# Kernel optimization log

Hardware: AMD Instinct MI355X
Metric: run time of the kernel (lower is better)

## Reference

```python
import jax, jax.numpy as jnp
import numpy as np

B, CIN, H, W = 4, 2048, 65, 65
NC, INNER, QL = 19, 256, 2975
TEMP = 0.2
EPS = 1e-5


def _conv(x, w, dil=1, pad=0):
    return jax.lax.conv_general_dilated(
        x, w, (1, 1), [(pad, pad), (pad, pad)], rhs_dilation=(dil, dil),
        dimension_numbers=('NCHW', 'OIHW', 'NCHW'))


def _bn_relu(x, g, b):
    # training-mode BatchNorm2d (batch statistics over N,H,W) + ReLU
    m = x.mean(axis=(0, 2, 3), keepdims=True)
    v = x.var(axis=(0, 2, 3), keepdims=True)
    return jax.nn.relu(g[None, :, None, None] * (x - m) * jax.lax.rsqrt(v + EPS)
                       + b[None, :, None, None])


def setup_inputs() -> dict:
    key = jax.random.key(0)
    ks = jax.random.split(key, 12)
    rn = lambda k, s, sc=0.02: jax.random.normal(k, s, jnp.float32) * sc
    inp = {
        'x': jax.random.normal(ks[0], (B, CIN, H, W), jnp.float32),
        # ASPP: global-pool branch (1x1), 1x1 branch, three dilated 3x3 branches
        'w_gp': rn(ks[1], (INNER, CIN, 1, 1)), 'g_gp': jnp.ones(INNER), 'b_gp': jnp.zeros(INNER),
        'w_1x1': rn(ks[2], (INNER, CIN, 1, 1)), 'g_1x1': jnp.ones(INNER), 'b_1x1': jnp.zeros(INNER),
        'w_d12': rn(ks[3], (INNER, CIN, 3, 3)), 'g_d12': jnp.ones(INNER), 'b_d12': jnp.zeros(INNER),
        'w_d24': rn(ks[4], (INNER, CIN, 3, 3)), 'g_d24': jnp.ones(INNER), 'b_d24': jnp.zeros(INNER),
        'w_d36': rn(ks[5], (INNER, CIN, 3, 3)), 'g_d36': jnp.ones(INNER), 'b_d36': jnp.zeros(INNER),
        # head: 3x3 conv on 5*INNER concat -> 256, BN, ReLU (Dropout2d = identity)
        'w_head': rn(ks[6], (256, 5 * INNER, 3, 3)), 'g_head': jnp.ones(256), 'b_head': jnp.zeros(256),
        # final 1x1 classifier
        'w_fin': rn(ks[7], (NC, 256, 1, 1)), 'b_fin': jnp.zeros(NC),
    }
    q = jax.random.normal(ks[8], (NC, INNER, QL), jnp.float32)
    inp['queues'] = q / jnp.linalg.norm(q, axis=1, keepdims=True)  # normalize dim=0 per-class
    return inp


def reference(x, w_gp, g_gp, b_gp, w_1x1, g_1x1, b_1x1,
              w_d12, g_d12, b_d12, w_d24, g_d24, b_d24, w_d36, g_d36, b_d36,
              w_head, g_head, b_head, w_fin, b_fin, queues):
    bsz = x.shape[0]
    # ---- ASPP ----
    gp = x.mean(axis=(2, 3), keepdims=True)                       # global avg pool
    br0 = _bn_relu(_conv(gp, w_gp), g_gp, b_gp)
    br0 = jnp.broadcast_to(br0, (bsz, INNER, x.shape[2], x.shape[3]))
    br1 = _bn_relu(_conv(x, w_1x1), g_1x1, b_1x1)
    br2 = _bn_relu(_conv(x, w_d12, 12, 12), g_d12, b_d12)
    br3 = _bn_relu(_conv(x, w_d24, 24, 24), g_d24, b_d24)
    br4 = _bn_relu(_conv(x, w_d36, 36, 36), g_d36, b_d36)
    aspp_out = jnp.concatenate([br0, br1, br2, br3, br4], axis=1)  # (B, 5*INNER, H, W)
    # ---- head + final (Dropout2d(0.1) treated as identity) ----
    fea = _bn_relu(_conv(aspp_out, w_head, 1, 1), g_head, b_head)  # (B, 256, H, W)
    res = _conv(fea, w_fin) + b_fin[None, :, None, None]           # (B, NC, H, W)
    # ---- construct_region: per-class masked mean over ALL batch pixels ----
    pred = jnp.argmax(res, axis=1).reshape(bsz, -1)                # (B, HW)
    onehot = (pred[:, None, :] == jnp.arange(NC)[None, :, None]).astype(fea.dtype)  # (B,NC,HW)
    feaf = fea.reshape(bsz, 256, -1)                               # (B, 256, HW)
    sums = jnp.einsum('bcp,bkp->kc', feaf, onehot)                 # (NC, 256)
    counts = onehot.sum(axis=(0, 2))                               # (NC,)
    keys = sums / jnp.maximum(counts, 1.0)[:, None]
    keys = keys / jnp.maximum(jnp.linalg.norm(keys, axis=1, keepdims=True), 1e-12)
    present = counts > 0
    # ---- contrast loss: (query . queue)/INNER == mean over channels ----
    sims = jnp.einsum('kc,jcl->kjl', keys, jax.lax.stop_gradient(queues)) / INNER  # (NC,NC,QL)
    a = sims / TEMP
    lse_rows = jax.nn.logsumexp(a, axis=2)                         # (NC, NC)
    neg_rows = jnp.where(jnp.eye(NC, dtype=bool), -jnp.inf, lse_rows)
    lse_neg = jax.nn.logsumexp(neg_rows, axis=1)                   # (NC,) lse over 18*QL negatives
    pos = a[jnp.arange(NC), jnp.arange(NC)]                        # (NC, QL) diagonal class sims
    # CE with label 0 over [pos_i, negs] == logaddexp(pos_i, lse_neg) - pos_i, averaged over QL
    loss_per = (jnp.logaddexp(pos, lse_neg[:, None]) - pos).mean(axis=1)
    contrast_loss = jnp.sum(jnp.where(present, loss_per, 0.0))
    return res, contrast_loss
```

## Files before the change

kernel.cpp:

```cpp
#include <hip/hip_runtime.h>
#include <stdint.h>

#define HW_   4225
#define NPIX_ 16900
#define NC_   19
#define QL_   2975
#define EPSF  1e-5f

typedef __bf16 bf16x8 __attribute__((ext_vector_type(8)));
typedef float  f32x4  __attribute__((ext_vector_type(4)));

__device__ __forceinline__ unsigned short f2bf(float f) {
    union { float f; unsigned u; } v; v.f = f;
    unsigned u = v.u;
    return (unsigned short)((u + 0x7fffu + ((u >> 16) & 1u)) >> 16);
}
__device__ __forceinline__ float bf2f(unsigned short b) {
    union { unsigned u; float f; } v; v.u = ((unsigned)b) << 16;
    return v.f;
}

__global__ void k_transpose_x(const float* __restrict__ x, unsigned short* __restrict__ xt) {
    __shared__ unsigned short T[64][66];
    int b  = blockIdx.z;
    int c0 = blockIdx.y * 64;
    int p0 = blockIdx.x * 64;
    int tx = threadIdx.x & 63, ty = threadIdx.x >> 6;
    if (p0 + tx < HW_) {
        #pragma unroll
        for (int i = 0; i < 16; ++i) {
            int cl = i * 4 + ty;
            T[cl][tx] = f2bf(x[((size_t)(b * 2048 + c0 + cl)) * HW_ + p0 + tx]);
        }
    }
    __syncthreads();
    #pragma unroll
    for (int i = 0; i < 16; ++i) {
        int pl = i * 4 + ty;
        int p = p0 + pl;
        if (p < HW_) xt[((size_t)(b * HW_ + p)) * 2048 + c0 + tx] = T[tx][pl];
    }
}

__global__ void k_gp(const float* __restrict__ x, float* __restrict__ gp) {
    int wid  = blockIdx.x * 4 + (threadIdx.x >> 6);
    int lane = threadIdx.x & 63;
    int b = wid >> 11, c = wid & 2047;
    const float* src = x + (size_t)(b * 2048 + c) * HW_;
    float s = 0.f;
    for (int i = lane; i < HW_; i += 64) s += src[i];
    #pragma unroll
    for (int off = 32; off; off >>= 1) s += __shfl_down(s, off);
    if (lane == 0) gp[b * 2048 + c] = s * (1.0f / HW_);
}

__global__ void k_wreorder(const float* __restrict__ src, unsigned short* __restrict__ dst,
                           int ci_n, int ntaps) {
    int ci  = blockIdx.x * 256 + threadIdx.x;
    int co  = blockIdx.y, tap = blockIdx.z;
    dst[((size_t)tap * 256 + co) * ci_n + ci] =
        f2bf(src[((size_t)co * ci_n + ci) * ntaps + tap]);
}

__global__ __launch_bounds__(256) void k_conv_gemm(
    const unsigned short* __restrict__ xin, const unsigned short* __restrict__ wr_base,
    unsigned short* __restrict__ out, int cin, int ostride, int is_head)
{
    __shared__ unsigned short As[128 * 72];
    __shared__ unsigned short Bs[128 * 72];
    const int tid = threadIdx.x;
    const int bz = blockIdx.z;
    int dil, ntaps, coff;
    if (is_head) { dil = 1; ntaps = 9; coff = 0; }
    else         { dil = 12 * bz; ntaps = bz ? 9 : 1; coff = 256 * (bz + 1); }
    const int mbase = blockIdx.x * 128;
    const int nbase = blockIdx.y * 128;

    const int srow = tid >> 1;
    const int scol = (tid & 1) << 5;

    const int pix = mbase + srow;
    const int pb = pix / HW_;
    const int pr = pix - pb * HW_;
    const int py = pr / 65;
    const int px = pr - py * 65;

    f32x4 acc[4][4];
    #pragma unroll
    for (int i = 0; i < 4; ++i)
        #pragma unroll
        for (int j = 0; j < 4; ++j) acc[i][j] = (f32x4){0.f, 0.f, 0.f, 0.f};

    const int wv = tid >> 6, lane = tid & 63;
    const int wm = wv >> 1, wn = wv & 1;
    const int quad = lane >> 4, lrow = lane & 15;

    for (int tap = 0; tap < ntaps; ++tap) {
        int dy = (ntaps == 1) ? 0 : (tap / 3 - 1) * dil;
        int dx = (ntaps == 1) ? 0 : (tap % 3 - 1) * dil;
        int ys = py + dy, xs = px + dx;
        bool valid = (pix < NPIX_) && ((unsigned)ys < 65u) && ((unsigned)xs < 65u);
        size_t aoff = valid ? ((size_t)(pb * HW_ + ys * 65 + xs) * cin + scol) : 0;
        const unsigned short* asrc = xin + aoff;
        const unsigned short* bsrc = wr_base +
            ((size_t)(bz * 9 + tap) * 256 + (nbase + srow)) * cin + scol;

        for (int kc = 0; kc < cin; kc += 64) {
            uint4 a0, a1, a2, a3;
            if (valid) {
                const uint4* ap = (const uint4*)(asrc + kc);
                a0 = ap[0]; a1 = ap[1]; a2 = ap[2]; a3 = ap[3];
            } else {
                a0 = a1 = a2 = a3 = make_uint4(0u, 0u, 0u, 0u);
            }
            const uint4* bp = (const uint4*)(bsrc + kc);
            uint4 b0 = bp[0], b1 = bp[1], b2 = bp[2], b3 = bp[3];
            __syncthreads();
            uint4* ad = (uint4*)(As + srow * 72 + scol);
            ad[0] = a0; ad[1] = a1; ad[2] = a2; ad[3] = a3;
            uint4* bd = (uint4*)(Bs + srow * 72 + scol);
            bd[0] = b0; bd[1] = b1; bd[2] = b2; bd[3] = b3;
            __syncthreads();

            #pragma unroll
            for (int kk = 0; kk < 64; kk += 32) {
                const int ko = kk + (quad << 3);
                bf16x8 af[4], bfv[4];
                #pragma unroll
                for (int i = 0; i < 4; ++i)
                    af[i] = *(const bf16x8*)(As + (wm * 64 + i * 16 + lrow) * 72 + ko);
                #pragma unroll
                for (int j = 0; j < 4; ++j)
                    bfv[j] = *(const bf16x8*)(Bs + (wn * 64 + j * 16 + lrow) * 72 + ko);
                #pragma unroll
                for (int i = 0; i < 4; ++i)
                    #pragma unroll
                    for (int j = 0; j < 4; ++j)
                        acc[i][j] = __builtin_amdgcn_mfma_f32_16x16x32_bf16(
                            af[i], bfv[j], acc[i][j], 0, 0, 0);
            }
        }
    }

    #pragma unroll
    for (int i = 0; i < 4; ++i) {
        int prow = mbase + wm * 64 + i * 16 + quad * 4;
        #pragma unroll
        for (int r = 0; r < 4; ++r) {
            int p = prow + r;
            if (p < NPIX_) {
                unsigned short* orow = out + (size_t)p * ostride + coff + nbase + wn * 64 + lrow;
                #pragma unroll
                for (int j = 0; j < 4; ++j) orow[j * 16] = f2bf(acc[i][j][r]);
            }
        }
    }
}

__global__ void k_stats(const unsigned short* __restrict__ buf, int stride, int coff,
                        float* __restrict__ sums, float* __restrict__ sumsq) {
    int c = blockIdx.y * 256 + threadIdx.x;
    int p0 = blockIdx.x * 130, p1 = p0 + 130;
    float s = 0.f, q = 0.f;
    for (int p = p0; p < p1; ++p) {
        float v = bf2f(buf[(size_t)p * stride + coff + c]);
        s += v; q += v * v;
    }
    atomicAdd(&sums[c], s);
    atomicAdd(&sumsq[c], q);
}

__global__ void k_br0mv(const float* __restrict__ gp, const float* __restrict__ wgp,
                        float* __restrict__ pre) {
    __shared__ float red[256];
    int co = blockIdx.x, t = threadIdx.x;
    float s0 = 0, s1 = 0, s2 = 0, s3 = 0;
    for (int ci = t; ci < 2048; ci += 256) {
        float w = wgp[(size_t)co * 2048 + ci];
        s0 += w * gp[ci];        s1 += w * gp[2048 + ci];
        s2 += w * gp[4096 + ci]; s3 += w * gp[6144 + ci];
    }
    #pragma unroll
    for (int b = 0; b < 4; ++b) {
        float s = (b == 0) ? s0 : (b == 1) ? s1 : (b == 2) ? s2 : s3;
        red[t] = s; __syncthreads();
        for (int st = 128; st; st >>= 1) { if (t < st) red[t] += red[t + st]; __syncthreads(); }
        if (t == 0) pre[b * 256 + co] = red[0];
        __syncthreads();
    }
}

__global__ void k_br0bn(const float* __restrict__ pre, const float* __restrict__ g,
                        const float* __restrict__ bb, float* __restrict__ post) {
    int t = threadIdx.x;
    float v0 = pre[t], v1 = pre[256 + t], v2 = pre[512 + t], v3 = pre[768 + t];
    float m = 0.25f * (v0 + v1 + v2 + v3);
    float var = 0.25f * (v0 * v0 + v1 * v1 + v2 * v2 + v3 * v3) - m * m;
    float sc = g[t] * rsqrtf(var + EPSF), sh = bb[t] - m * sc;
    post[t]       = fmaxf(v0 * sc + sh, 0.f);
    post[256 + t] = fmaxf(v1 * sc + sh, 0.f);
    post[512 + t] = fmaxf(v2 * sc + sh, 0.f);
    post[768 + t] = fmaxf(v3 * sc + sh, 0.f);
}

__global__ void k_norm_aspp(unsigned short* __restrict__ buf,
                            const float* __restrict__ sums, const float* __restrict__ sumsq,
                            const float* __restrict__ g1, const float* __restrict__ b1,
                            const float* __restrict__ g2, const float* __restrict__ b2,
                            const float* __restrict__ g3, const float* __restrict__ b3,
                            const float* __restrict__ g4, const float* __restrict__ b4,
                            const float* __restrict__ br0) {
    int cg = blockIdx.y, t = threadIdx.x;
    int p0 = blockIdx.x * 130, p1 = p0 + 130;
    if (cg == 0) {
        for (int p = p0; p < p1; ++p) {
            int b = p / HW_;
            buf[(size_t)p * 1280 + t] = f2bf(br0[b * 256 + t]);
        }
    } else {
        int c = (cg - 1) * 256 + t;
        float m = sums[c] * (1.f / NPIX_);
        float var = sumsq[c] * (1.f / NPIX_) - m * m;
        const float* g  = (cg == 1) ? g1 : (cg == 2) ? g2 : (cg == 3) ? g3 : g4;
        const float* bb = (cg == 1) ? b1 : (cg == 2) ? b2 : (cg == 3) ? b3 : b4;
        float sc = g[t] * rsqrtf(var + EPSF), sh = bb[t] - m * sc;
        for (int p = p0; p < p1; ++p) {
            size_t idx = (size_t)p * 1280 + cg * 256 + t;
            float v = bf2f(buf[idx]) * sc + sh;
            buf[idx] = f2bf(fmaxf(v, 0.f));
        }
    }
}

__global__ void k_norm_head(unsigned short* __restrict__ buf,
                            const float* __restrict__ sums, const float* __restrict__ sumsq,
                            const float* __restrict__ g, const float* __restrict__ bb) {
    int t = threadIdx.x;
    float m = sums[t] * (1.f / NPIX_);
    float var = sumsq[t] * (1.f / NPIX_) - m * m;
    float sc = g[t] * rsqrtf(var + EPSF), sh = bb[t] - m * sc;
    int p0 = blockIdx.x * 130, p1 = p0 + 130;
    for (int p = p0; p < p1; ++p) {
        size_t idx = (size_t)p * 256 + t;
        float v = bf2f(buf[idx]) * sc + sh;
        buf[idx] = f2bf(fmaxf(v, 0.f));
    }
}

__global__ void k_final(const unsigned short* __restrict__ fea, const float* __restrict__ wfin,
                        const float* __restrict__ bfin, float* __restrict__ outres) {
    int idx = blockIdx.x * 256 + threadIdx.x;
    if (idx >= NPIX_ * NC_) return;
    int p = idx / NC_, k = idx - p * NC_;
    const unsigned short* f = fea + (size_t)p * 256;
    const float* w = wfin + k * 256;
    float acc = 0.f;
    for (int c = 0; c < 256; c += 8) {
        uint4 q = *(const uint4*)(f + c);
        unsigned u0 = q.x, u1 = q.y, u2 = q.z, u3 = q.w;
        acc += bf2f((unsigned short)(u0 & 0xffff)) * w[c + 0];
        acc += bf2f((unsigned short)(u0 >> 16))    * w[c + 1];
        acc += bf2f((unsigned short)(u1 & 0xffff)) * w[c + 2];
        acc += bf2f((unsigned short)(u1 >> 16))    * w[c + 3];
        acc += bf2f((unsigned short)(u2 & 0xffff)) * w[c + 4];
        acc += bf2f((unsigned short)(u2 >> 16))    * w[c + 5];
        acc += bf2f((unsigned short)(u3 & 0xffff)) * w[c + 6];
        acc += bf2f((unsigned short)(u3 >> 16))    * w[c + 7];
    }
    acc += bfin[k];
    int b = p / HW_, yx = p - b * HW_;
    outres[(size_t)(b * NC_ + k) * HW_ + yx] = acc;
}

__global__ void k_argmax(const float* __restrict__ res, int* __restrict__ pred) {
    int p = blockIdx.x * 256 + threadIdx.x;
    if (p >= NPIX_) return;
    int b = p / HW_, yx = p - b * HW_;
    const float* r = res + (size_t)b * NC_ * HW_ + yx;
    float best = r[0]; int bi = 0;
    #pragma unroll
    for (int k = 1; k < NC_; ++k) {
        float v = r[(size_t)k * HW_];
        if (v > best) { best = v; bi = k; }
    }
    pred[p] = bi;
}

__global__ void k_keysums(const unsigned short* __restrict__ fea, const int* __restrict__ pred,
                          float* __restrict__ sums, float* __restrict__ counts) {
    __shared__ float acc[256 * NC_];
    __shared__ float cnt[NC_];
    int t = threadIdx.x;
    #pragma unroll
    for (int k = 0; k < NC_; ++k) acc[t * NC_ + k] = 0.f;
    if (t < NC_) cnt[t] = 0.f;
    __syncthreads();
    int p0 = blockIdx.x * 130, p1 = p0 + 130;
    for (int p = p0; p < p1; ++p) {
        int k = pred[p];
        float v = bf2f(fea[(size_t)p * 256 + t]);
        acc[t * NC_ + k] += v;
        if (t == 0) cnt[k] += 1.f;
    }
    __syncthreads();
    #pragma unroll
    for (int k = 0; k < NC_; ++k) atomicAdd(&sums[k * 256 + t], acc[t * NC_ + k]);
    if (t < NC_) atomicAdd(&counts[t], cnt[t]);
}

__global__ void k_keys(const float* __restrict__ sums, const float* __restrict__ counts,
                       float* __restrict__ keys) {
    __shared__ float red[256];
    int t = threadIdx.x;
    for (int k = 0; k < NC_; ++k) {
        float v = sums[k * 256 + t] / fmaxf(counts[k], 1.f);
        red[t] = v * v; __syncthreads();
        for (int s = 128; s; s >>= 1) { if (t < s) red[t] += red[t + s]; __syncthreads(); }
        float inv = 1.f / fmaxf(sqrtf(red[0]), 1e-12f);
        keys[k * 256 + t] = v * inv;
        __syncthreads();
    }
}

__global__ void k_sims(const float* __restrict__ keys, const float* __restrict__ queues,
                       float* __restrict__ Sexp, float* __restrict__ pos_a) {
    __shared__ float kl[NC_ * 256];
    __shared__ float red[256];
    int t = threadIdx.x;
    int j = blockIdx.x, lc = blockIdx.y;
    #pragma unroll
    for (int k = 0; k < NC_; ++k) kl[k * 256 + t] = keys[k * 256 + t];
    __syncthreads();
    int l = lc * 256 + t;
    bool lv = l < QL_;
    float a[NC_];
    #pragma unroll
    for (int k = 0; k < NC_; ++k) a[k] = 0.f;
    if (lv) {
        const float* q = queues + (size_t)j * 256 * QL_ + l;
        for (int c = 0; c < 256; ++c) {
            float qv = q[(size_t)c * QL_];
            #pragma unroll
            for (int k = 0; k < NC_; ++k) a[k] += kl[k * 256 + c] * qv;
        }
    }
    const float invt = 1.f / (256.f * 0.2f);
    if (lv) pos_a[j * QL_ + l] = a[j] * invt;
    for (int k = 0; k < NC_; ++k) {
        float e = lv ? __expf(a[k] * invt) : 0.f;
        red[t] = e; __syncthreads();
        for (int s = 128; s; s >>= 1) { if (t < s) red[t] += red[t + s]; __syncthreads(); }
        if (t == 0) atomicAdd(&Sexp[k * NC_ + j], red[0]);
        __syncthreads();
    }
}

__global__ void k_loss(const float* __restrict__ Sexp, const float* __restrict__ pos_a,
                       const float* __restrict__ counts, float* __restrict__ out_loss) {
    __shared__ float red[256];
    __shared__ float lseneg[NC_];
    int t = threadIdx.x;
    if (t < NC_) {
        float s = 0.f;
        for (int j = 0; j < NC_; ++j) if (j != t) s += Sexp[t * NC_ + j];
        lseneg[t] = logf(s);
    }
    __syncthreads();
    float total = 0.f;
    for (int k = 0; k < NC_; ++k) {
        float L = lseneg[k];
        float s = 0.f;
        for (int l = t; l < QL_; l += 256) {
            float pos = pos_a[k * QL_ + l];
            float m = fmaxf(pos, L);
            s += logf(__expf(pos - m) + __expf(L - m)) + m - pos;
        }
        red[t] = s; __syncthreads();
        for (int st = 128; st; st >>= 1) { if (t < st) red[t] += red[t + st]; __syncthreads(); }
        if (t == 0 && counts[k] > 0.f) total += red[0] * (1.f / QL_);
        __syncthreads();
    }
    if (t == 0) *out_loss = total;
}

extern "C" void kernel_launch(void* const* d_in, const int* in_sizes, int n_in,
                              void* d_out, int out_size, void* d_ws, size_t ws_size,
                              hipStream_t stream) {
    const float* x      = (const float*)d_in[0];
    const float* w_gp   = (const float*)d_in[1];
    const float* g_gp   = (const float*)d_in[2];
    const float* b_gp   = (const float*)d_in[3];
    const float* w_1x1  = (const float*)d_in[4];
    const float* g_1x1  = (const float*)d_in[5];
    const float* b_1x1  = (const float*)d_in[6];
    const float* w_d12  = (const float*)d_in[7];
    const float* g_d12  = (const float*)d_in[8];
    const float* b_d12  = (const float*)d_in[9];
    const float* w_d24  = (const float*)d_in[10];
    const float* g_d24  = (const float*)d_in[11];
    const float* b_d24  = (const float*)d_in[12];
    const float* w_d36  = (const float*)d_in[13];
    const float* g_d36  = (const float*)d_in[14];
    const float* b_d36  = (const float*)d_in[15];
    const float* w_head = (const float*)d_in[16];
    const float* g_head = (const float*)d_in[17];
    const float* b_head = (const float*)d_in[18];
    const float* w_fin  = (const float*)d_in[19];
    const float* b_fin  = (const float*)d_in[20];
    const float* queues = (const float*)d_in[21];

    char* ws = (char*)d_ws;
    size_t off = 0;
    auto alloc = [&](size_t bytes) { void* p = ws + off; off += (bytes + 255) & ~(size_t)255; return p; };

    unsigned short* x_t     = (unsigned short*)alloc((size_t)4 * HW_ * 2048 * 2);
    unsigned short* wr_aspp = (unsigned short*)alloc((size_t)4 * 9 * 256 * 2048 * 2);
    unsigned short* wr_head = (unsigned short*)alloc((size_t)9 * 256 * 1280 * 2);
    unsigned short* aspp    = (unsigned short*)alloc((size_t)NPIX_ * 1280 * 2);
    unsigned short* headb   = (unsigned short*)alloc((size_t)NPIX_ * 256 * 2);
    float* gp      = (float*)alloc(8192 * 4);
    float* br0pre  = (float*)alloc(1024 * 4);
    float* br0post = (float*)alloc(1024 * 4);
    int*   pred    = (int*)alloc((size_t)NPIX_ * 4);
    float* pos_a   = (float*)alloc((size_t)NC_ * QL_ * 4);
    float* zbase      = (float*)alloc(7808 * 4);
    float* aspp_sums  = zbase;
    float* aspp_sumsq = zbase + 1024;
    float* head_sums  = zbase + 2048;
    float* head_sumsq = zbase + 2304;
    float* key_sums   = zbase + 2560;
    float* counts     = zbase + 7424;
    float* Sexp       = zbase + 7443;
    (void)ws_size; (void)in_sizes; (void)n_in; (void)out_size;

    float* res  = (float*)d_out;
    float* loss = (float*)d_out + (size_t)NPIX_ * NC_;

    hipMemsetAsync(zbase, 0, 7808 * 4, stream);

    k_transpose_x<<<dim3(67, 32, 4), 256, 0, stream>>>(x, x_t);
    k_gp<<<2048, 256, 0, stream>>>(x, gp);

    k_wreorder<<<dim3(8, 256, 1), 256, 0, stream>>>(w_1x1, wr_aspp, 2048, 1);
    k_wreorder<<<dim3(8, 256, 9), 256, 0, stream>>>(w_d12, wr_aspp + (size_t)1 * 9 * 256 * 2048, 2048, 9);
    k_wreorder<<<dim3(8, 256, 9), 256, 0, stream>>>(w_d24, wr_aspp + (size_t)2 * 9 * 256 * 2048, 2048, 9);
    k_wreorder<<<dim3(8, 256, 9), 256, 0, stream>>>(w_d36, wr_aspp + (size_t)3 * 9 * 256 * 2048, 2048, 9);
    k_wreorder<<<dim3(5, 256, 9), 256, 0, stream>>>(w_head, wr_head, 1280, 9);

    k_conv_gemm<<<dim3(133, 2, 4), 256, 0, stream>>>(x_t, wr_aspp, aspp, 2048, 1280, 0);

    k_stats<<<dim3(130, 4), 256, 0, stream>>>(aspp, 1280, 256, aspp_sums, aspp_sumsq);
    k_br0mv<<<256, 256, 0, stream>>>(gp, w_gp, br0pre);
    k_br0bn<<<1, 256, 0, stream>>>(br0pre, g_gp, b_gp, br0post);
    k_norm_aspp<<<dim3(130, 5), 256, 0, stream>>>(aspp, aspp_sums, aspp_sumsq,
        g_1x1, b_1x1, g_d12, b_d12, g_d24, b_d24, g_d36, b_d36, br0post);

    k_conv_gemm<<<dim3(133, 2, 1), 256, 0, stream>>>(aspp, wr_head, headb, 1280, 256, 1);
    k_stats<<<dim3(130, 1), 256, 0, stream>>>(headb, 256, 0, head_sums, head_sumsq);
    k_norm_head<<<130, 256, 0, stream>>>(headb, head_sums, head_sumsq, g_head, b_head);

    k_final<<<(NPIX_ * NC_ + 255) / 256, 256, 0, stream>>>(headb, w_fin, b_fin, res);
    k_argmax<<<(NPIX_ + 255) / 256, 256, 0, stream>>>(res, pred);
    k_keysums<<<130, 256, 0, stream>>>(headb, pred, key_sums, counts);
    k_keys<<<1, 256, 0, stream>>>(key_sums, counts, (float*)br0pre );
    k_sims<<<dim3(NC_, 12), 256, 0, stream>>>((float*)br0pre, queues, Sexp, pos_a);
    k_loss<<<1, 256, 0, stream>>>(Sexp, pos_a, counts, loss);
}
```

Before: 1.667 ms.

## Use direct global-to-LDS loads with XOR swizzle, skip empty taps, fuse global pooling

The conv GEMM now stages A and B tiles with global_load_lds directly into an XOR-swizzled LDS layout, dropping the register round trip and the padded stride. Invalid rows read from a zero page instead of branching. Taps where no pixel in the tile is valid are skipped. The global average pool is folded into the transpose kernel through atomics, which removes a separate full pass over x. The costs are extra barriers per tap, atomic contention on the pooled sums, and a global-to-LDS path with no double buffering.

```diff
diff --git a/kernel.cpp b/kernel.cpp
--- a/kernel.cpp
+++ b/kernel.cpp
@@ -7,6 +7,9 @@
 #define QL_   2975
 #define EPSF  1e-5f
 
+#define AS1 __attribute__((address_space(1)))
+#define AS3 __attribute__((address_space(3)))
+
 typedef __bf16 bf16x8 __attribute__((ext_vector_type(8)));
 typedef float  f32x4  __attribute__((ext_vector_type(4)));
 
@@ -20,38 +23,36 @@
     return v.f;
 }
 
-__global__ void k_transpose_x(const float* __restrict__ x, unsigned short* __restrict__ xt) {
-    __shared__ unsigned short T[64][66];
+__global__ void k_transpose_x(const float* __restrict__ x, unsigned short* __restrict__ xt,
+                              float* __restrict__ gp_acc) {
+    __shared__ float T[64][66];
+    __shared__ float red[256];
     int b  = blockIdx.z;
     int c0 = blockIdx.y * 64;
     int p0 = blockIdx.x * 64;
     int tx = threadIdx.x & 63, ty = threadIdx.x >> 6;
-    if (p0 + tx < HW_) {
-        #pragma unroll
-        for (int i = 0; i < 16; ++i) {
-            int cl = i * 4 + ty;
-            T[cl][tx] = f2bf(x[((size_t)(b * 2048 + c0 + cl)) * HW_ + p0 + tx]);
-        }
+    bool pv = (p0 + tx) < HW_;
+    #pragma unroll
+    for (int i = 0; i < 16; ++i) {
+        int cl = i * 4 + ty;
+        T[cl][tx] = pv ? x[((size_t)(b * 2048 + c0 + cl)) * HW_ + p0 + tx] : 0.f;
     }
     __syncthreads();
     #pragma unroll
     for (int i = 0; i < 16; ++i) {
         int pl = i * 4 + ty;
         int p = p0 + pl;
-        if (p < HW_) xt[((size_t)(b * HW_ + p)) * 2048 + c0 + tx] = T[tx][pl];
-    }
-}
-
-__global__ void k_gp(const float* __restrict__ x, float* __restrict__ gp) {
-    int wid  = blockIdx.x * 4 + (threadIdx.x >> 6);
-    int lane = threadIdx.x & 63;
-    int b = wid >> 11, c = wid & 2047;
-    const float* src = x + (size_t)(b * 2048 + c) * HW_;
+        if (p < HW_) xt[((size_t)(b * HW_ + p)) * 2048 + c0 + tx] = f2bf(T[tx][pl]);
+    }
     float s = 0.f;
-    for (int i = lane; i < HW_; i += 64) s += src[i];
-    #pragma unroll
-    for (int off = 32; off; off >>= 1) s += __shfl_down(s, off);
-    if (lane == 0) gp[b * 2048 + c] = s * (1.0f / HW_);
+    #pragma unroll
+    for (int k = 0; k < 16; ++k) s += T[tx][ty * 16 + k];
+    red[threadIdx.x] = s;
+    __syncthreads();
+    if (threadIdx.x < 64) {
+        float t = red[threadIdx.x] + red[64 + threadIdx.x] + red[128 + threadIdx.x] + red[192 + threadIdx.x];
+        atomicAdd(&gp_acc[b * 2048 + c0 + threadIdx.x], t);
+    }
 }
 
 __global__ void k_wreorder(const float* __restrict__ src, unsigned short* __restrict__ dst,
@@ -64,10 +65,12 @@
 
 __global__ __launch_bounds__(256) void k_conv_gemm(
     const unsigned short* __restrict__ xin, const unsigned short* __restrict__ wr_base,
-    unsigned short* __restrict__ out, int cin, int ostride, int is_head)
+    unsigned short* __restrict__ out, const unsigned short* __restrict__ zp,
+    int cin, int ostride, int is_head)
 {
-    __shared__ unsigned short As[128 * 72];
-    __shared__ unsigned short Bs[128 * 72];
+    __shared__ unsigned short As[128 * 64];
+    __shared__ unsigned short Bs[128 * 64];
+    __shared__ int tapvalid;
     const int tid = threadIdx.x;
     const int bz = blockIdx.z;
     int dil, ntaps, coff;
@@ -76,14 +79,24 @@
     const int mbase = blockIdx.x * 128;
     const int nbase = blockIdx.y * 128;
 
-    const int srow = tid >> 1;
-    const int scol = (tid & 1) << 5;
-
-    const int pix = mbase + srow;
-    const int pb = pix / HW_;
-    const int pr = pix - pb * HW_;
-    const int py = pr / 65;
-    const int px = pr - py * 65;
+    const int wv = tid >> 6, lane = tid & 63;
+    const int wm = wv >> 1, wn = wv & 1;
+    const int quad = lane >> 4, lrow = lane & 15;
+    const int sw = lrow & 7;
+
+    const int rowoff = lane >> 3;
+    const int lchunk = (lane & 7) ^ rowoff;
+
+    int py4[4], px4[4], pb4[4], pix4[4];
+    #pragma unroll
+    for (int q = 0; q < 4; ++q) {
+        int r = 32 * wv + 8 * q + rowoff;
+        int pix = mbase + r;
+        pix4[q] = pix;
+        int pb = pix / HW_;
+        int pr = pix - pb * HW_;
+        py4[q] = pr / 65; px4[q] = pr - py4[q] * 65; pb4[q] = pb;
+    }
 
     f32x4 acc[4][4];
     #pragma unroll
@@ -91,47 +104,57 @@
         #pragma unroll
         for (int j = 0; j < 4; ++j) acc[i][j] = (f32x4){0.f, 0.f, 0.f, 0.f};
 
-    const int wv = tid >> 6, lane = tid & 63;
-    const int wm = wv >> 1, wn = wv & 1;
-    const int quad = lane >> 4, lrow = lane & 15;
-
     for (int tap = 0; tap < ntaps; ++tap) {
         int dy = (ntaps == 1) ? 0 : (tap / 3 - 1) * dil;
         int dx = (ntaps == 1) ? 0 : (tap % 3 - 1) * dil;
-        int ys = py + dy, xs = px + dx;
-        bool valid = (pix < NPIX_) && ((unsigned)ys < 65u) && ((unsigned)xs < 65u);
-        size_t aoff = valid ? ((size_t)(pb * HW_ + ys * 65 + xs) * cin + scol) : 0;
-        const unsigned short* asrc = xin + aoff;
-        const unsigned short* bsrc = wr_base +
-            ((size_t)(bz * 9 + tap) * 256 + (nbase + srow)) * cin + scol;
+
+        const unsigned short* aptr[4];
+        const unsigned short* bptr[4];
+        bool av[4];
+        bool anyv = false;
+        #pragma unroll
+        for (int q = 0; q < 4; ++q) {
+            int ys = py4[q] + dy, xs = px4[q] + dx;
+            bool v = (pix4[q] < NPIX_) && ((unsigned)ys < 65u) && ((unsigned)xs < 65u);
+            av[q] = v; anyv |= v;
+            aptr[q] = v ? (xin + ((size_t)(pb4[q] * HW_ + ys * 65 + xs)) * cin + lchunk * 8) : zp;
+            bptr[q] = wr_base + ((size_t)((bz * 9 + tap) * 256 + nbase + 32 * wv + 8 * q + rowoff)) * cin + lchunk * 8;
+        }
+
+        if (tid == 0) tapvalid = 0;
+        __syncthreads();
+        if (anyv) tapvalid = 1;
+        __syncthreads();
+        if (!tapvalid) continue;
 
         for (int kc = 0; kc < cin; kc += 64) {
-            uint4 a0, a1, a2, a3;
-            if (valid) {
-                const uint4* ap = (const uint4*)(asrc + kc);
-                a0 = ap[0]; a1 = ap[1]; a2 = ap[2]; a3 = ap[3];
-            } else {
-                a0 = a1 = a2 = a3 = make_uint4(0u, 0u, 0u, 0u);
+            __syncthreads();
+            #pragma unroll
+            for (int q = 0; q < 4; ++q) {
+                const unsigned short* pa = av[q] ? (aptr[q] + kc) : zp;
+                __builtin_amdgcn_global_load_lds(
+                    (const AS1 void*)pa,
+                    (AS3 void*)(As + (32 * wv + 8 * q) * 64), 16, 0, 0);
+                __builtin_amdgcn_global_load_lds(
+                    (const AS1 void*)(bptr[q] + kc),
+                    (AS3 void*)(Bs + (32 * wv + 8 * q) * 64), 16, 0, 0);
             }
-            const uint4* bp = (const uint4*)(bsrc + kc);
-            uint4 b0 = bp[0], b1 = bp[1], b2 = bp[2], b3 = bp[3];
             __syncthreads();
-            uint4* ad = (uint4*)(As + srow * 72 + scol);
-            ad[0] = a0; ad[1] = a1; ad[2] = a2; ad[3] = a3;
-            uint4* bd = (uint4*)(Bs + srow * 72 + scol);
-            bd[0] = b0; bd[1] = b1; bd[2] = b2; bd[3] = b3;
-            __syncthreads();
 
             #pragma unroll
-            for (int kk = 0; kk < 64; kk += 32) {
-                const int ko = kk + (quad << 3);
+            for (int kk = 0; kk < 2; ++kk) {
+                const int koch = kk * 4 + quad;
                 bf16x8 af[4], bfv[4];
                 #pragma unroll
-                for (int i = 0; i < 4; ++i)
-                    af[i] = *(const bf16x8*)(As + (wm * 64 + i * 16 + lrow) * 72 + ko);
+                for (int i = 0; i < 4; ++i) {
+                    int row = wm * 64 + i * 16 + lrow;
+                    af[i] = *(const bf16x8*)(As + row * 64 + ((koch ^ sw) << 3));
+                }
                 #pragma unroll
-                for (int j = 0; j < 4; ++j)
-                    bfv[j] = *(const bf16x8*)(Bs + (wn * 64 + j * 16 + lrow) * 72 + ko);
+                for (int j = 0; j < 4; ++j) {
+                    int row = wn * 64 + j * 16 + lrow;
+                    bfv[j] = *(const bf16x8*)(Bs + row * 64 + ((koch ^ sw) << 3));
+                }
                 #pragma unroll
                 for (int i = 0; i < 4; ++i)
                     #pragma unroll
@@ -185,7 +208,7 @@
         float s = (b == 0) ? s0 : (b == 1) ? s1 : (b == 2) ? s2 : s3;
         red[t] = s; __syncthreads();
         for (int st = 128; st; st >>= 1) { if (t < st) red[t] += red[t + st]; __syncthreads(); }
-        if (t == 0) pre[b * 256 + co] = red[0];
+        if (t == 0) pre[b * 256 + co] = red[0] * (1.0f / HW_);
         __syncthreads();
     }
 }
@@ -418,28 +441,28 @@
     unsigned short* wr_head = (unsigned short*)alloc((size_t)9 * 256 * 1280 * 2);
     unsigned short* aspp    = (unsigned short*)alloc((size_t)NPIX_ * 1280 * 2);
     unsigned short* headb   = (unsigned short*)alloc((size_t)NPIX_ * 256 * 2);
-    float* gp      = (float*)alloc(8192 * 4);
     float* br0pre  = (float*)alloc(1024 * 4);
     float* br0post = (float*)alloc(1024 * 4);
     int*   pred    = (int*)alloc((size_t)NPIX_ * 4);
     float* pos_a   = (float*)alloc((size_t)NC_ * QL_ * 4);
-    float* zbase      = (float*)alloc(7808 * 4);
-    float* aspp_sums  = zbase;
-    float* aspp_sumsq = zbase + 1024;
-    float* head_sums  = zbase + 2048;
-    float* head_sumsq = zbase + 2304;
-    float* key_sums   = zbase + 2560;
-    float* counts     = zbase + 7424;
-    float* Sexp       = zbase + 7443;
+    float* zbase       = (float*)alloc(16060 * 4);
+    unsigned short* zp = (unsigned short*)zbase;
+    float* gp          = zbase + 64;
+    float* aspp_sums   = zbase + 8256;
+    float* aspp_sumsq  = zbase + 9280;
+    float* head_sums   = zbase + 10304;
+    float* head_sumsq  = zbase + 10560;
+    float* key_sums    = zbase + 10816;
+    float* counts      = zbase + 15680;
+    float* Sexp        = zbase + 15699;
     (void)ws_size; (void)in_sizes; (void)n_in; (void)out_size;
 
     float* res  = (float*)d_out;
     float* loss = (float*)d_out + (size_t)NPIX_ * NC_;
 
-    hipMemsetAsync(zbase, 0, 7808 * 4, stream);
-
-    k_transpose_x<<<dim3(67, 32, 4), 256, 0, stream>>>(x, x_t);
-    k_gp<<<2048, 256, 0, stream>>>(x, gp);
+    hipMemsetAsync(zbase, 0, 16060 * 4, stream);
+
+    k_transpose_x<<<dim3(67, 32, 4), 256, 0, stream>>>(x, x_t, gp);
 
     k_wreorder<<<dim3(8, 256, 1), 256, 0, stream>>>(w_1x1, wr_aspp, 2048, 1);
     k_wreorder<<<dim3(8, 256, 9), 256, 0, stream>>>(w_d12, wr_aspp + (size_t)1 * 9 * 256 * 2048, 2048, 9);
@@ -447,7 +470,7 @@
     k_wreorder<<<dim3(8, 256, 9), 256, 0, stream>>>(w_d36, wr_aspp + (size_t)3 * 9 * 256 * 2048, 2048, 9);
     k_wreorder<<<dim3(5, 256, 9), 256, 0, stream>>>(w_head, wr_head, 1280, 9);
 
-    k_conv_gemm<<<dim3(133, 2, 4), 256, 0, stream>>>(x_t, wr_aspp, aspp, 2048, 1280, 0);
+    k_conv_gemm<<<dim3(133, 2, 4), 256, 0, stream>>>(x_t, wr_aspp, aspp, zp, 2048, 1280, 0);
 
     k_stats<<<dim3(130, 4), 256, 0, stream>>>(aspp, 1280, 256, aspp_sums, aspp_sumsq);
     k_br0mv<<<256, 256, 0, stream>>>(gp, w_gp, br0pre);
@@ -455,14 +478,14 @@
     k_norm_aspp<<<dim3(130, 5), 256, 0, stream>>>(aspp, aspp_sums, aspp_sumsq,
         g_1x1, b_1x1, g_d12, b_d12, g_d24, b_d24, g_d36, b_d36, br0post);
 
-    k_conv_gemm<<<dim3(133, 2, 1), 256, 0, stream>>>(aspp, wr_head, headb, 1280, 256, 1);
+    k_conv_gemm<<<dim3(133, 2, 1), 256, 0, stream>>>(aspp, wr_head, headb, zp, 1280, 256, 1);
     k_stats<<<dim3(130, 1), 256, 0, stream>>>(headb, 256, 0, head_sums, head_sumsq);
     k_norm_head<<<130, 256, 0, stream>>>(headb, head_sums, head_sumsq, g_head, b_head);
 
     k_final<<<(NPIX_ * NC_ + 255) / 256, 256, 0, stream>>>(headb, w_fin, b_fin, res);
     k_argmax<<<(NPIX_ + 255) / 256, 256, 0, stream>>>(res, pred);
     k_keysums<<<130, 256, 0, stream>>>(headb, pred, key_sums, counts);
-    k_keys<<<1, 256, 0, stream>>>(key_sums, counts, (float*)br0pre );
+    k_keys<<<1, 256, 0, stream>>>(key_sums, counts, (float*)br0pre);
     k_sims<<<dim3(NC_, 12), 256, 0, stream>>>((float*)br0pre, queues, Sexp, pos_a);
     k_loss<<<1, 256, 0, stream>>>(Sexp, pos_a, counts, loss);
 }
```

After: 1.405 ms. -15.7%, faster.
